# Optimization experiments

Measured on AMD Instinct MI355X. Metric: run time of the kernel, lower is better.

The kernel has to match this reference:

```python
import jax, jax.numpy as jnp
import numpy as np

CH = 16      # channel_n
HID = 128    # hidden_n


def _max_pool3(a):
    # a: [B,1,H,W]; 3x3 max pool, stride 1, padding 1 (matches F.max_pool2d)
    return jax.lax.reduce_window(
        a, -jnp.inf, jax.lax.max,
        window_dimensions=(1, 1, 3, 3),
        window_strides=(1, 1, 1, 1),
        padding=((0, 0), (0, 0), (1, 1), (1, 1)))


def _living_mask(x):
    return _max_pool3(x[:, 3:4]) > 0.1


def _nca_step(x, perceive_w, w1, b1, w2, key):
    pre_life = _living_mask(x)                                  # [B,1,H,W] bool
    # depthwise sobel conv, identical weight layout/groups as torch Conv2d(groups=CH)
    p = jax.lax.conv_general_dilated(
        x, perceive_w, window_strides=(1, 1),
        padding=((1, 1), (1, 1)),
        dimension_numbers=('NCHW', 'OIHW', 'NCHW'),
        feature_group_count=CH)                                  # [B,2*CH,H,W]
    comb = jnp.transpose(jnp.concatenate([x, p], axis=1), (0, 2, 3, 1))  # [B,H,W,3*CH]
    h = jax.nn.relu(comb @ w1 + b1)                              # [B,H,W,HID]
    delta = jnp.transpose(h @ w2, (0, 3, 1, 2))                  # [B,CH,H,W]
    alpha = x[:, 3:4]
    upd = (jax.random.uniform(key, alpha.shape, dtype=x.dtype) < 0.5) & (alpha > 0.1)
    x = x + delta * upd.astype(x.dtype)
    life = pre_life & _living_mask(x)
    return x * life.astype(x.dtype)


def setup_inputs() -> dict:
    key = jax.random.key(0)
    kx, k1, k2 = jax.random.split(key, 3)
    B, H, W = 2, 128, 128
    x = jax.random.uniform(kx, (B, CH, H, W), dtype=jnp.float32)
    sobel_x = jnp.array([[-1., 0., 1.], [-2., 0., 2.], [-1., 0., 1.]], dtype=jnp.float32)
    sobel_y = jnp.array([[-1., -2., -1.], [0., 0., 0.], [1., 2., 1.]], dtype=jnp.float32)
    wx = jnp.tile(sobel_x[None, None], (CH, 1, 1, 1))
    wy = jnp.tile(sobel_y[None, None], (CH, 1, 1, 1))
    perceive_w = jnp.concatenate([wx, wy], axis=0)               # [2*CH,1,3,3]
    w1 = jax.random.normal(k1, (CH * 3, HID), dtype=jnp.float32) * 0.02
    b1 = jnp.zeros((HID,), dtype=jnp.float32)
    w2 = jax.random.normal(k2, (HID, CH), dtype=jnp.float32) * 0.02
    return {"x": x, "perceive_w": perceive_w, "w1": w1, "b1": b1, "w2": w2, "steps": 64}


def reference(x, perceive_w, w1, b1, w2, steps):
    keys = jax.random.split(jax.random.key(42), steps)

    def body(carry, k):
        return _nca_step(carry, perceive_w, w1, b1, w2, k), None

    x, _ = jax.lax.scan(body, x, keys)
    return x
```

## Files before the change

### kernel.cpp

```cpp
#include <hip/hip_runtime.h>
#include <stdint.h>

#define HH 128
#define WW 128
#define CHN 16
#define NPIX (HH*WW)
#define PLANE (CHN*NPIX)
#define STEPS 64
#define TW 8
#define TH 8

__host__ __device__ __forceinline__ uint32_t rotl32_(uint32_t x, int d) {
  return (x << d) | (x >> (32 - d));
}

__host__ __device__ __forceinline__ void tf2x32(uint32_t k0, uint32_t k1,
                                                uint32_t x0, uint32_t x1,
                                                uint32_t* o0, uint32_t* o1) {
  uint32_t ks0 = k0, ks1 = k1, ks2 = k0 ^ k1 ^ 0x1BD11BDAu;
  x0 += ks0; x1 += ks1;
  x0 += x1; x1 = rotl32_(x1, 13); x1 ^= x0;
  x0 += x1; x1 = rotl32_(x1, 15); x1 ^= x0;
  x0 += x1; x1 = rotl32_(x1, 26); x1 ^= x0;
  x0 += x1; x1 = rotl32_(x1, 6);  x1 ^= x0;
  x0 += ks1; x1 += ks2 + 1u;
  x0 += x1; x1 = rotl32_(x1, 17); x1 ^= x0;
  x0 += x1; x1 = rotl32_(x1, 29); x1 ^= x0;
  x0 += x1; x1 = rotl32_(x1, 16); x1 ^= x0;
  x0 += x1; x1 = rotl32_(x1, 24); x1 ^= x0;
  x0 += ks2; x1 += ks0 + 2u;
  x0 += x1; x1 = rotl32_(x1, 13); x1 ^= x0;
  x0 += x1; x1 = rotl32_(x1, 15); x1 ^= x0;
  x0 += x1; x1 = rotl32_(x1, 26); x1 ^= x0;
  x0 += x1; x1 = rotl32_(x1, 6);  x1 ^= x0;
  x0 += ks0; x1 += ks1 + 3u;
  x0 += x1; x1 = rotl32_(x1, 17); x1 ^= x0;
  x0 += x1; x1 = rotl32_(x1, 29); x1 ^= x0;
  x0 += x1; x1 = rotl32_(x1, 16); x1 ^= x0;
  x0 += x1; x1 = rotl32_(x1, 24); x1 ^= x0;
  x0 += ks1; x1 += ks2 + 4u;
  x0 += x1; x1 = rotl32_(x1, 13); x1 ^= x0;
  x0 += x1; x1 = rotl32_(x1, 15); x1 ^= x0;
  x0 += x1; x1 = rotl32_(x1, 26); x1 ^= x0;
  x0 += x1; x1 = rotl32_(x1, 6);  x1 ^= x0;
  x0 += ks2; x1 += ks0 + 5u;
  *o0 = x0; *o1 = x1;
}

__global__ void prep_w1t(const float* __restrict__ w1, float* __restrict__ w1t) {
  int i = blockIdx.x * 256 + threadIdx.x;
  if (i < 48 * 128) {
    int j = i / 48, k = i % 48;
    w1t[i] = w1[k * 128 + j];
  }
}

__global__ __launch_bounds__(256, 2) void nca_step1(
    const float* __restrict__ xin, const float* __restrict__ pw,
    const float* __restrict__ w1t, const float* __restrict__ b1,
    const float* __restrict__ w2, float* __restrict__ xtld,
    float* __restrict__ prelife, uint32_t k0, uint32_t k1)
{
  __shared__ float xt[CHN][TH + 2][TW + 2];
  __shared__ float dbuf[3][64][17];

  const int tid = threadIdx.x;
  const int bx = blockIdx.x;
  const int by = blockIdx.y;
  const int b  = blockIdx.z;
  const int h0 = by * TH, w0 = bx * TW;

  const float* xb = xin + (size_t)b * PLANE;
  for (int i = tid; i < CHN * (TH + 2) * (TW + 2); i += 256) {
    int c  = i / ((TH + 2) * (TW + 2));
    int r  = (i / (TW + 2)) % (TH + 2);
    int cc = i % (TW + 2);
    int gh = h0 + r - 1, gw = w0 + cc - 1;
    float v = 0.f;
    if (gh >= 0 && gh < HH && gw >= 0 && gw < WW) v = xb[(c * HH + gh) * WW + gw];
    xt[c][r][cc] = v;
  }
  __syncthreads();

  const int wv   = __builtin_amdgcn_readfirstlane((int)threadIdx.x) >> 6;
  const int lane = tid & 63;
  const int pr = lane >> 3, pc = lane & 7;
  const int jbase = wv * 32;

  float comb[48];
  float premax = -1e30f;
  #pragma unroll
  for (int c = 0; c < CHN; ++c) {
    float n[9];
    #pragma unroll
    for (int dy = 0; dy < 3; ++dy)
      #pragma unroll
      for (int dx = 0; dx < 3; ++dx)
        n[dy * 3 + dx] = xt[c][pr + dy][pc + dx];
    comb[c] = n[4];
    float p0 = 0.f, p1 = 0.f;
    #pragma unroll
    for (int i = 0; i < 9; ++i) {
      p0 = fmaf(pw[(2 * c) * 9 + i], n[i], p0);
      p1 = fmaf(pw[(2 * c + 1) * 9 + i], n[i], p1);
    }
    comb[16 + 2 * c] = p0;
    comb[17 + 2 * c] = p1;
    if (c == 3) {
      float m = n[0];
      #pragma unroll
      for (int i = 1; i < 9; ++i) m = fmaxf(m, n[i]);
      premax = m;
    }
  }
  #pragma unroll
  for (int k = 0; k < 48; ++k) asm volatile("" : "+v"(comb[k]));

  float delta[16];
  #pragma unroll
  for (int c = 0; c < 16; ++c) delta[c] = 0.f;
  for (int jj = 0; jj < 32; jj += 2) {
    const int j0 = jbase + jj;
    const float* wr0 = w1t + j0 * 48;
    const float* wr1 = wr0 + 48;
    float h0 = b1[j0], h1 = b1[j0 + 1];
    #pragma unroll
    for (int k = 0; k < 48; ++k) {
      h0 = fmaf(comb[k], wr0[k], h0);
      h1 = fmaf(comb[k], wr1[k], h1);
    }
    h0 = fmaxf(h0, 0.f); h1 = fmaxf(h1, 0.f);
    const float* w20 = w2 + j0 * 16;
    const float* w21 = w20 + 16;
    #pragma unroll
    for (int c = 0; c < 16; ++c)
      delta[c] = fmaf(h0, w20[c], fmaf(h1, w21[c], delta[c]));
  }

  if (wv) {
    #pragma unroll
    for (int c = 0; c < 16; ++c) dbuf[wv - 1][lane][c] = delta[c];
  }
  __syncthreads();
  if (wv == 0) {
    #pragma unroll
    for (int t = 0; t < 3; ++t)
      #pragma unroll
      for (int c = 0; c < 16; ++c) delta[c] += dbuf[t][lane][c];

    const int gh = h0 + pr, gw = w0 + pc;
    const int gidx = gh * WW + gw;

    uint32_t o0, o1;
    tf2x32(k0, k1, 0u, (uint32_t)(b * NPIX + gidx), &o0, &o1);
    const uint32_t bits = o0 ^ o1;
    const float u = (((bits >> 31) == 0u) && (comb[3] > 0.1f)) ? 1.f : 0.f;

    float* qb = xtld + (size_t)b * PLANE;
    #pragma unroll
    for (int c = 0; c < CHN; ++c)
      qb[c * NPIX + gidx] = fmaf(delta[c], u, comb[c]);
    prelife[b * NPIX + gidx] = (premax > 0.1f) ? 1.f : 0.f;
  }
}

__global__ __launch_bounds__(256) void nca_step2(
    const float* __restrict__ xtld, const float* __restrict__ prelife,
    float* __restrict__ xout)
{
  const int g = blockIdx.x * 256 + threadIdx.x;
  const int b = g >> 14, hw = g & (NPIX - 1);
  const int h = hw >> 7, w = hw & 127;
  const float* qb = xtld + (size_t)b * PLANE;
  const float* ap = qb + 3 * NPIX;
  float m = -1e30f;
  #pragma unroll
  for (int dy = -1; dy <= 1; ++dy) {
    int hh = h + dy; if (hh < 0 || hh >= HH) continue;
    #pragma unroll
    for (int dx = -1; dx <= 1; ++dx) {
      int ww2 = w + dx; if (ww2 < 0 || ww2 >= WW) continue;
      m = fmaxf(m, ap[hh * WW + ww2]);
    }
  }
  const float life = (m > 0.1f && prelife[g] > 0.5f) ? 1.f : 0.f;
  float* ob = xout + (size_t)b * PLANE;
  #pragma unroll
  for (int c = 0; c < CHN; ++c)
    ob[c * NPIX + hw] = qb[c * NPIX + hw] * life;
}

extern "C" void kernel_launch(void* const* d_in, const int* in_sizes, int n_in,
                              void* d_out, int out_size, void* d_ws, size_t ws_size,
                              hipStream_t stream) {
  (void)in_sizes; (void)n_in; (void)out_size; (void)ws_size;
  const float* x  = (const float*)d_in[0];
  const float* pw = (const float*)d_in[1];
  const float* w1 = (const float*)d_in[2];
  const float* b1 = (const float*)d_in[3];
  const float* w2 = (const float*)d_in[4];

  float* out = (float*)d_out;
  float* ws  = (float*)d_ws;
  float* bufQ    = ws;
  float* prelife = ws + 2 * PLANE;
  float* w1t     = ws + 2 * PLANE + 2 * NPIX;

  prep_w1t<<<(48 * 128 + 255) / 256, 256, 0, stream>>>(w1, w1t);

  uint32_t key0[STEPS], key1[STEPS];
  for (uint32_t s = 0; s < STEPS; ++s)
    tf2x32(0u, 42u, 0u, s, &key0[s], &key1[s]);

  dim3 g1(WW / TW, HH / TH, 2);
  for (int s = 0; s < STEPS; ++s) {
    const float* src = (s == 0) ? x : out;
    nca_step1<<<g1, 256, 0, stream>>>(src, pw, w1t, b1, w2, bufQ, prelife,
                                      key0[s], key1[s]);
    nca_step2<<<(2 * NPIX) / 256, 256, 0, stream>>>(bufQ, prelife, out);
  }
}
```

Measured before the change: 1.418 ms.

## Fuse life-mask pass into next step kernel with ping-pong buffers

The separate post-step masking kernel is removed. Each step kernel now recomputes the previous step's living mask from a 2-pixel alpha halo and the stored pre-life map, then applies it to the loaded tile, so a trailing final kernel is needed only once. This halves the kernel launches and cuts a full read/write pass over the state per step, at the cost of redundant halo max-pool work and extra shared memory. The hidden-layer loop now computes four units per iteration, and the cross-wave reduction and output stores are spread across all four waves instead of being done by wave 0 alone.

```diff
diff --git a/kernel.cpp b/kernel.cpp
--- a/kernel.cpp
+++ b/kernel.cpp
@@ -55,29 +55,64 @@
   }
 }
 
+template <int MASKED>
 __global__ __launch_bounds__(256, 2) void nca_step1(
-    const float* __restrict__ xin, const float* __restrict__ pw,
-    const float* __restrict__ w1t, const float* __restrict__ b1,
-    const float* __restrict__ w2, float* __restrict__ xtld,
-    float* __restrict__ prelife, uint32_t k0, uint32_t k1)
+    const float* __restrict__ xin, const float* __restrict__ plin,
+    const float* __restrict__ pw, const float* __restrict__ w1t,
+    const float* __restrict__ b1, const float* __restrict__ w2,
+    float* __restrict__ xtld, float* __restrict__ plout,
+    uint32_t k0, uint32_t k1)
 {
   __shared__ float xt[CHN][TH + 2][TW + 2];
-  __shared__ float dbuf[3][64][17];
+  __shared__ float At[TH + 4][TW + 4];
+  __shared__ float Lf[TH + 2][TW + 2];
+  __shared__ float dbuf[4][64][17];
 
   const int tid = threadIdx.x;
   const int bx = blockIdx.x;
   const int by = blockIdx.y;
   const int b  = blockIdx.z;
-  const int h0 = by * TH, w0 = bx * TW;
-
+  const int oh = by * TH, ow = bx * TW;
   const float* xb = xin + (size_t)b * PLANE;
+
+  if (MASKED) {
+    for (int i = tid; i < (TH + 4) * (TW + 4); i += 256) {
+      int r = i / (TW + 4), cc = i % (TW + 4);
+      int gh = oh + r - 2, gw = ow + cc - 2;
+      float v = 0.f;
+      if (gh >= 0 && gh < HH && gw >= 0 && gw < WW)
+        v = xb[(3 * HH + gh) * WW + gw];
+      At[r][cc] = v;
+    }
+    __syncthreads();
+    for (int i = tid; i < (TH + 2) * (TW + 2); i += 256) {
+      int r = i / (TW + 2), cc = i % (TW + 2);
+      int gh = oh + r - 1, gw = ow + cc - 1;
+      float life = 0.f;
+      if (gh >= 0 && gh < HH && gw >= 0 && gw < WW) {
+        float m = At[r][cc];
+        m = fmaxf(m, At[r][cc + 1]); m = fmaxf(m, At[r][cc + 2]);
+        m = fmaxf(m, At[r + 1][cc]); m = fmaxf(m, At[r + 1][cc + 1]);
+        m = fmaxf(m, At[r + 1][cc + 2]);
+        m = fmaxf(m, At[r + 2][cc]); m = fmaxf(m, At[r + 2][cc + 1]);
+        m = fmaxf(m, At[r + 2][cc + 2]);
+        if (m > 0.1f && plin[b * NPIX + gh * WW + gw] > 0.5f) life = 1.f;
+      }
+      Lf[r][cc] = life;
+    }
+    __syncthreads();
+  }
+
   for (int i = tid; i < CHN * (TH + 2) * (TW + 2); i += 256) {
     int c  = i / ((TH + 2) * (TW + 2));
     int r  = (i / (TW + 2)) % (TH + 2);
     int cc = i % (TW + 2);
-    int gh = h0 + r - 1, gw = w0 + cc - 1;
+    int gh = oh + r - 1, gw = ow + cc - 1;
     float v = 0.f;
-    if (gh >= 0 && gh < HH && gw >= 0 && gw < WW) v = xb[(c * HH + gh) * WW + gw];
+    if (gh >= 0 && gh < HH && gw >= 0 && gw < WW) {
+      v = xb[(c * HH + gh) * WW + gw];
+      if (MASKED) v *= Lf[r][cc];
+    }
     xt[c][r][cc] = v;
   }
   __syncthreads();
@@ -119,52 +154,59 @@
   float delta[16];
   #pragma unroll
   for (int c = 0; c < 16; ++c) delta[c] = 0.f;
-  for (int jj = 0; jj < 32; jj += 2) {
+  for (int jj = 0; jj < 32; jj += 4) {
     const int j0 = jbase + jj;
-    const float* wr0 = w1t + j0 * 48;
-    const float* wr1 = wr0 + 48;
-    float h0 = b1[j0], h1 = b1[j0 + 1];
+    const float* wr = w1t + j0 * 48;
+    float a0 = b1[j0], a1 = b1[j0 + 1], a2 = b1[j0 + 2], a3 = b1[j0 + 3];
     #pragma unroll
     for (int k = 0; k < 48; ++k) {
-      h0 = fmaf(comb[k], wr0[k], h0);
-      h1 = fmaf(comb[k], wr1[k], h1);
-    }
-    h0 = fmaxf(h0, 0.f); h1 = fmaxf(h1, 0.f);
+      const float ck = comb[k];
+      a0 = fmaf(ck, wr[k], a0);
+      a1 = fmaf(ck, wr[k + 48], a1);
+      a2 = fmaf(ck, wr[k + 96], a2);
+      a3 = fmaf(ck, wr[k + 144], a3);
+    }
+    a0 = fmaxf(a0, 0.f); a1 = fmaxf(a1, 0.f);
+    a2 = fmaxf(a2, 0.f); a3 = fmaxf(a3, 0.f);
     const float* w20 = w2 + j0 * 16;
-    const float* w21 = w20 + 16;
-    #pragma unroll
-    for (int c = 0; c < 16; ++c)
-      delta[c] = fmaf(h0, w20[c], fmaf(h1, w21[c], delta[c]));
-  }
-
-  if (wv) {
-    #pragma unroll
-    for (int c = 0; c < 16; ++c) dbuf[wv - 1][lane][c] = delta[c];
-  }
+    #pragma unroll
+    for (int c = 0; c < 16; ++c) {
+      float d = delta[c];
+      d = fmaf(a0, w20[c], d);
+      d = fmaf(a1, w20[16 + c], d);
+      d = fmaf(a2, w20[32 + c], d);
+      d = fmaf(a3, w20[48 + c], d);
+      delta[c] = d;
+    }
+  }
+
+  #pragma unroll
+  for (int c = 0; c < 16; ++c) dbuf[wv][lane][c] = delta[c];
   __syncthreads();
-  if (wv == 0) {
-    #pragma unroll
-    for (int t = 0; t < 3; ++t)
-      #pragma unroll
-      for (int c = 0; c < 16; ++c) delta[c] += dbuf[t][lane][c];
-
-    const int gh = h0 + pr, gw = w0 + pc;
-    const int gidx = gh * WW + gw;
-
-    uint32_t o0, o1;
-    tf2x32(k0, k1, 0u, (uint32_t)(b * NPIX + gidx), &o0, &o1);
-    const uint32_t bits = o0 ^ o1;
-    const float u = (((bits >> 31) == 0u) && (comb[3] > 0.1f)) ? 1.f : 0.f;
-
-    float* qb = xtld + (size_t)b * PLANE;
-    #pragma unroll
-    for (int c = 0; c < CHN; ++c)
-      qb[c * NPIX + gidx] = fmaf(delta[c], u, comb[c]);
-    prelife[b * NPIX + gidx] = (premax > 0.1f) ? 1.f : 0.f;
-  }
-}
-
-__global__ __launch_bounds__(256) void nca_step2(
+
+  const int cb = wv * 4;
+  const int gh = oh + pr, gw = ow + pc;
+  const int gidx = gh * WW + gw;
+
+  uint32_t o0, o1;
+  tf2x32(k0, k1, 0u, (uint32_t)(b * NPIX + gidx), &o0, &o1);
+  const uint32_t bits = o0 ^ o1;
+  const float u = (((bits >> 31) == 0u) && (comb[3] > 0.1f)) ? 1.f : 0.f;
+
+  float* qb = xtld + (size_t)b * PLANE;
+  #pragma unroll
+  for (int c2 = 0; c2 < 4; ++c2) {
+    const int c = cb + c2;
+    float s = delta[c];
+    #pragma unroll
+    for (int t = 0; t < 4; ++t)
+      if (t != wv) s += dbuf[t][lane][c];
+    qb[c * NPIX + gidx] = fmaf(s, u, comb[c]);
+  }
+  if (wv == 0) plout[b * NPIX + gidx] = (premax > 0.1f) ? 1.f : 0.f;
+}
+
+__global__ __launch_bounds__(256) void nca_final(
     const float* __restrict__ xtld, const float* __restrict__ prelife,
     float* __restrict__ xout)
 {
@@ -174,10 +216,8 @@
   const float* qb = xtld + (size_t)b * PLANE;
   const float* ap = qb + 3 * NPIX;
   float m = -1e30f;
-  #pragma unroll
   for (int dy = -1; dy <= 1; ++dy) {
     int hh = h + dy; if (hh < 0 || hh >= HH) continue;
-    #pragma unroll
     for (int dx = -1; dx <= 1; ++dx) {
       int ww2 = w + dx; if (ww2 < 0 || ww2 >= WW) continue;
       m = fmaxf(m, ap[hh * WW + ww2]);
@@ -202,9 +242,9 @@
 
   float* out = (float*)d_out;
   float* ws  = (float*)d_ws;
-  float* bufQ    = ws;
-  float* prelife = ws + 2 * PLANE;
-  float* w1t     = ws + 2 * PLANE + 2 * NPIX;
+  float* xbuf[2] = { ws, ws + 2 * PLANE };
+  float* pbuf[2] = { ws + 4 * PLANE, ws + 4 * PLANE + 2 * NPIX };
+  float* w1t     = ws + 4 * PLANE + 4 * NPIX;
 
   prep_w1t<<<(48 * 128 + 255) / 256, 256, 0, stream>>>(w1, w1t);
 
@@ -213,10 +253,13 @@
     tf2x32(0u, 42u, 0u, s, &key0[s], &key1[s]);
 
   dim3 g1(WW / TW, HH / TH, 2);
-  for (int s = 0; s < STEPS; ++s) {
-    const float* src = (s == 0) ? x : out;
-    nca_step1<<<g1, 256, 0, stream>>>(src, pw, w1t, b1, w2, bufQ, prelife,
-                                      key0[s], key1[s]);
-    nca_step2<<<(2 * NPIX) / 256, 256, 0, stream>>>(bufQ, prelife, out);
-  }
-}
+  nca_step1<0><<<g1, 256, 0, stream>>>(x, nullptr, pw, w1t, b1, w2,
+                                       xbuf[0], pbuf[0], key0[0], key1[0]);
+  for (int s = 1; s < STEPS; ++s) {
+    const int pv = (s - 1) & 1, cu = s & 1;
+    nca_step1<1><<<g1, 256, 0, stream>>>(xbuf[pv], pbuf[pv], pw, w1t, b1, w2,
+                                         xbuf[cu], pbuf[cu], key0[s], key1[s]);
+  }
+  const int lf = (STEPS - 1) & 1;
+  nca_final<<<(2 * NPIX) / 256, 256, 0, stream>>>(xbuf[lf], pbuf[lf], out);
+}
```

After: 1.731 ms. 1.22x slower.
